# Performance work log

Measured on AMD Instinct MI355X. Metric: run time of the kernel, lower is better.

## Reference

```python
import jax, jax.numpy as jnp
import numpy as np

D_MODEL = 1024; D_STATE = 64; HEADDIM = 64; EXPAND = 2
D_INNER = EXPAND * D_MODEL            # 2048
NHEADS = D_INNER // HEADDIM           # 32
NGROUPS = 1
GN = NGROUPS * D_STATE                # 64
CONV_DIM = D_INNER + 2 * (2 * GN)     # 2304
D_IN_PROJ = 2 * D_INNER + 2 * (2 * GN) + 2 * NHEADS  # 4416
K_SP = 7; K_TP = 4; CHUNK = 256
BATCH = 2; FRAMES = 8; SPATIAL = 256; SEQLEN = SPATIAL * FRAMES  # 2048


def silu(x):
    return x * jax.nn.sigmoid(x)


def flip_frames(x, f):
    # 'b (l f) d -> b l f d' flip frame axis, flatten back
    b, L, d = x.shape
    return x.reshape(b, L // f, f, d)[:, :, ::-1, :].reshape(b, L, d)


def depthwise_conv1d(x, w, b, pad):
    # x: (N, L, C), w: (C, K) depthwise, pad=(lo,hi) -> (N, L_out, C)
    y = jax.lax.conv_general_dilated(
        jnp.transpose(x, (0, 2, 1)), w[:, None, :], (1,), [pad],
        feature_group_count=w.shape[0])
    return jnp.transpose(y + b[None, :, None], (0, 2, 1))


def setup_inputs():
    rng = np.random.default_rng(0)
    f32 = lambda *s: jnp.asarray(rng.standard_normal(s), jnp.float32)
    # dt_bias init exactly as in the torch module
    dt = np.exp(rng.random(NHEADS) * (np.log(0.1) - np.log(0.001)) + np.log(0.001))
    dt = np.clip(dt, 1e-4, None)
    inv_dt = dt + np.log(-np.expm1(-dt))
    return {
        "u": f32(BATCH, SEQLEN, D_MODEL),
        "in_proj_w": f32(D_IN_PROJ, D_MODEL) * 0.02,
        "conv_sp_w": f32(CONV_DIM, K_SP) * 0.2,
        "conv_sp_b": f32(CONV_DIM) * 0.02,
        "conv_tp_w": f32(CONV_DIM, K_TP) * 0.2,
        "conv_tp_b": f32(CONV_DIM) * 0.02,
        "dt_bias": jnp.asarray(inv_dt, jnp.float32),
        "A_log": jnp.zeros((NHEADS,), jnp.float32),
        "D": jnp.ones((NHEADS,), jnp.float32),
        "fc_D_w": f32(NHEADS, D_INNER) * 0.02,
        "norm_w": jnp.ones((D_INNER,), jnp.float32),
        "out_proj_w": f32(D_MODEL, D_INNER) * 0.02,
        "num_frames": FRAMES,
    }


def chunked_scan(xh, dt, A, Bm, Cm, sp, cs):
    # xh:(R,L,h,p) dt:(R,L,h) Bm,Cm:(R,L,n). ngroups=1.
    # seq_idx semantics: rows [0:b) one segment; rows [b:2b) reset every sp tokens.
    R, L, H, P = xh.shape
    nch = L // cs
    b = R // 2
    xch = xh.reshape(R, nch, cs, H, P)
    dtc = jnp.transpose(dt.reshape(R, nch, cs, H), (0, 1, 3, 2))   # (R,nch,h,cs)
    Bch = Bm.reshape(R, nch, cs, D_STATE)
    Cch = Cm.reshape(R, nch, cs, D_STATE)
    a = dtc * A[None, None, :, None]                               # negative logs
    cum = jnp.cumsum(a, axis=-1)                                   # inclusive
    mask = jnp.tril(jnp.ones((cs, cs), bool))
    seg = cum[..., :, None] - cum[..., None, :]                    # (R,nch,h,t,s)
    Lmat = jnp.where(mask, jnp.exp(jnp.where(mask, seg, 0.0)), 0.0)
    CB = jnp.einsum('rctn,rcsn->rcts', Cch, Bch)
    M = CB[:, :, None] * Lmat * dtc[:, :, :, None, :]
    Y_intra = jnp.einsum('rchts,rcshp->rcthp', M, xch)
    # chunk-final states and cross-chunk recurrence
    G = jnp.exp(cum[..., -1:] - cum) * dtc                         # (R,nch,h,cs)
    S_chunk = jnp.einsum('rchs,rcshp,rcsn->rchpn', G, xch, Bch)
    chunk_decay = jnp.exp(cum[..., -1])                            # (R,nch,h)
    cidx = jnp.arange(nch)
    rb = (cidx > 0) & ((cidx * cs) % sp == 0)
    resetc = jnp.concatenate([jnp.zeros((b, nch), bool),
                              jnp.broadcast_to(rb, (b, nch))], axis=0)

    def cstep(S, inp):
        dec, Sc, r = inp
        S = jnp.where(r[:, None, None, None], 0.0, S)
        prev = S
        S = dec[:, :, None, None] * S + Sc
        return S, prev

    S0 = jnp.zeros((R, H, P, D_STATE), xh.dtype)
    _, prevs = jax.lax.scan(
        cstep, S0,
        (jnp.transpose(chunk_decay, (1, 0, 2)),
         jnp.transpose(S_chunk, (1, 0, 2, 3, 4)),
         resetc.T))
    prev_states = jnp.transpose(prevs, (1, 0, 2, 3, 4))            # (R,nch,h,p,n)
    Y_inter = jnp.einsum('rcht,rctn,rchpn->rcthp', jnp.exp(cum), Cch, prev_states)
    return (Y_intra + Y_inter).reshape(R, L, H, P)


def reference(u, in_proj_w, conv_sp_w, conv_sp_b, conv_tp_w, conv_tp_b,
              dt_bias, A_log, D, fc_D_w, norm_w, out_proj_w, num_frames):
    batch, seqlen, _ = u.shape
    f = num_frames
    sp = seqlen // f
    zxbcdt = u @ in_proj_w.T
    z = zxbcdt[..., :D_INNER]
    xBC = zxbcdt[..., D_INNER:D_INNER + CONV_DIM]
    dt_raw = zxbcdt[..., D_INNER + CONV_DIM:]
    dt = jnp.concatenate([dt_raw[..., :NHEADS],
                          flip_frames(dt_raw[..., NHEADS:], f)], axis=0)
    dt = jax.nn.softplus(dt + dt_bias)                             # (2b,L,h)
    A = -jnp.exp(A_log)
    # spatial depthwise conv over spatial dim per frame ('same' pad) + SiLU
    xBC = xBC.reshape(batch, sp, f, CONV_DIM).transpose(0, 2, 1, 3).reshape(batch * f, sp, CONV_DIM)
    xBC = silu(depthwise_conv1d(xBC, conv_sp_w, conv_sp_b, (K_SP // 2, K_SP // 2)))
    # causal temporal depthwise conv over frame dim per spatial location + SiLU
    xBC = xBC.reshape(batch, f, sp, CONV_DIM).transpose(0, 2, 1, 3).reshape(batch * sp, f, CONV_DIM)
    xBC = silu(depthwise_conv1d(xBC, conv_tp_w, conv_tp_b, (K_TP - 1, 0)))
    xBC = xBC.reshape(batch, seqlen, CONV_DIM)
    x = xBC[..., :D_INNER]
    BC = xBC[..., D_INNER:]
    x_orig = x
    x2 = jnp.concatenate([x, flip_frames(x, f)], axis=0)
    BC2 = jnp.concatenate([BC[..., :2 * GN], flip_frames(BC[..., 2 * GN:], f)], axis=0)
    Bm, Cm = BC2[..., :GN], BC2[..., GN:]
    xh = x2.reshape(2 * batch, seqlen, NHEADS, HEADDIM)
    y = chunked_scan(xh, dt, A, Bm, Cm, sp, CHUNK)                 # (2b,L,h,p)
    y_fwd = y[:batch].reshape(batch, seqlen, D_INNER)
    y_rev = y[batch:].reshape(batch, sp, f, D_INNER)
    # roll-by-one with zeroed first position (fwd: token axis, rev: spatial axis)
    y_fwd = jnp.concatenate([jnp.zeros_like(y_fwd[:, :1]), y_fwd[:, :-1]], axis=1)
    y_rev = jnp.concatenate([jnp.zeros_like(y_rev[:, :1]), y_rev[:, :-1]], axis=1)
    y_rev = y_rev[:, :, ::-1, :].reshape(batch, seqlen, D_INNER)
    x_res = x_orig * jnp.repeat(x_orig @ fc_D_w.T + D, HEADDIM, axis=-1)
    y = y_fwd + y_rev + x_res
    # gated RMSNorm (norm_before_gate=True): rmsnorm(y)*w*silu(z)
    y = y * jax.lax.rsqrt(jnp.mean(jnp.square(y), axis=-1, keepdims=True) + 1e-5)
    y = y * norm_w * silu(z)
    return y @ out_proj_w.T
```

## Files before the change

kernel.cpp:

```cpp
#include <hip/hip_runtime.h>
#include <hip/hip_bf16.h>
#include <math.h>

#define D_STATE   64
#define HEADDIM   64
#define D_INNER   2048
#define NHEADS    32
#define GN        64
#define CONV_DIM  2304
#define D_IN_PROJ 4416
#define ZLD       4352
#define K_SP      7
#define K_TP      4
#define CHUNK     256
#define BATCHN    2
#define FRAMES    8
#define SPATIAL   256
#define SEQLEN    2048
#define NCH       8
#define MTOT      4096

typedef __attribute__((ext_vector_type(8))) short short8;
typedef __attribute__((ext_vector_type(8))) unsigned short ushort8v;
typedef __attribute__((ext_vector_type(4))) float floatx4;

__device__ __forceinline__ float silu_f(float x) { return x / (1.f + __expf(-x)); }
__device__ __forceinline__ int flip_l(int l) { return (l & ~7) | (7 - (l & 7)); }
__device__ __forceinline__ unsigned short f2bf(float f) {
  unsigned int u = __float_as_uint(f);
  unsigned int r = (u + 0x7fffu + ((u >> 16) & 1u)) >> 16;
  return (unsigned short)r;
}
__device__ __forceinline__ float bf2f(unsigned short s) {
  return __uint_as_float(((unsigned int)s) << 16);
}
__device__ __forceinline__ unsigned int cvtpk_bf16(float lo, float hi) {
  unsigned int r;
  asm("v_cvt_pk_bf16_f32 %0, %1, %2" : "=v"(r) : "v"(lo), "v"(hi));
  return r;
}
typedef union { short8 v; unsigned int u[4]; } s8u;
__device__ __forceinline__ void gload_lds16(const unsigned short* g, unsigned short* l) {
  __builtin_amdgcn_global_load_lds((const __attribute__((address_space(1))) void*)g,
                                   (__attribute__((address_space(3))) void*)l, 16, 0, 0);
}

__global__ __launch_bounds__(256) void cast4_bf16_kernel(const float* __restrict__ a,
                                                         unsigned short* __restrict__ oa,
                                                         int na,
                                                         const float* __restrict__ b,
                                                         unsigned short* __restrict__ ob,
                                                         int nb,
                                                         const float* __restrict__ c,
                                                         unsigned short* __restrict__ oc,
                                                         int nc,
                                                         const float* __restrict__ d,
                                                         unsigned short* __restrict__ od) {
  int bid = blockIdx.x;
  const float* in;
  unsigned short* out;
  size_t blk;
  if (bid < na)                 { in = a; out = oa; blk = bid; }
  else if (bid < na + nb)       { in = b; out = ob; blk = bid - na; }
  else if (bid < na + nb + nc)  { in = c; out = oc; blk = bid - na - nb; }
  else                          { in = d; out = od; blk = bid - na - nb - nc; }
  size_t i = (blk * 256 + threadIdx.x) * 4;
  float4 v = *(const float4*)(in + i);
  ushort4 o;
  o.x = f2bf(v.x); o.y = f2bf(v.y); o.z = f2bf(v.z); o.w = f2bf(v.w);
  *(ushort4*)(out + i) = o;
}

__device__ __forceinline__ void ts_body_bf16(const unsigned short* __restrict__ A, int lda,
                                             const unsigned short* __restrict__ B, int ldb,
                                             float* __restrict__ C, int ldc, int N, int K,
                                             int m0, float* red) {
  const int tid = threadIdx.x;
  const int lane = tid & 63;
  const int w = tid >> 6;
  const int fr = lane & 15;
  const int kq = (lane >> 4) * 8;
  const int nt = N >> 4;
  const int kseg = K >> 2;
  const int k0 = w * kseg;
  floatx4 acc[4] = {};
  for (int k = k0; k < k0 + kseg; k += 32) {
    short8 af = *(const short8*)(A + (size_t)(m0 + fr) * lda + k + kq);
    for (int j = 0; j < nt; ++j) {
      short8 bf8 = *(const short8*)(B + (size_t)(j * 16 + fr) * ldb + k + kq);
      acc[j] = __builtin_amdgcn_mfma_f32_16x16x32_bf16(af, bf8, acc[j], 0, 0, 0);
    }
  }
  const int rg = (lane >> 4) * 4;
  for (int j = 0; j < nt; ++j)
#pragma unroll
    for (int q = 0; q < 4; ++q)
      red[w * 1024 + j * 256 + (rg + q) * 16 + fr] = acc[j][q];
  __syncthreads();
  const int entries = nt * 256;
  for (int e = tid; e < entries; e += 256) {
    float s = red[e] + red[1024 + e] + red[2048 + e] + red[3072 + e];
    int j = e >> 8, idx = e & 255, row = idx >> 4, col = idx & 15;
    C[(size_t)(m0 + row) * ldc + j * 16 + col] = s;
  }
}

__global__ __launch_bounds__(256) void gemm_main_kernel(
    const unsigned short* __restrict__ A, int lda,
    const unsigned short* __restrict__ B, int ldb,
    unsigned short* __restrict__ C, int ldc, int K,
    const unsigned short* __restrict__ Bdt, float* __restrict__ DTraw) {
  __shared__ __align__(16) char smem[32768];
  const int tid = threadIdx.x;
  const int lane = tid & 63;
  const int w = tid >> 6;
  if (blockIdx.x >= 1088) {
    ts_body_bf16(A, lda, Bdt, lda, DTraw, 64, 64, K,
                 (blockIdx.x - 1088) * 16, (float*)smem);
    return;
  }
  unsigned short* As = (unsigned short*)smem;
  unsigned short* Bs = As + 128 * 64;
  const int bid = blockIdx.x;
  const int xcd = bid & 7;
  const int rp  = bid >> 3;
  const int px  = rp % 17;
  const int py  = rp / 17;
  const int m0 = ((xcd >> 1) * 8 + py) * 128;
  const int n0 = ((xcd & 1) * 17 + px) * 128;
  const int wm = (w >> 1) * 64;
  const int wn = (w & 1) * 64;
  const int lrow = lane >> 3;
  const int lperm = lane & 7;
  floatx4 acc[4][4] = {};
  for (int k0 = 0; k0 < K; k0 += 64) {
#pragma unroll
    for (int j = 0; j < 8; ++j) {
      int g = j * 4 + w;
      if (g < 16) {
        int row = g * 8 + lrow;
        int cg = (lperm ^ (row & 7)) * 8;
        gload_lds16(A + (size_t)(m0 + row) * lda + k0 + cg, &As[g * 512]);
      } else {
        int gb = g - 16;
        int row = gb * 8 + lrow;
        int cg = (lperm ^ (row & 7)) * 8;
        gload_lds16(B + (size_t)(n0 + row) * ldb + k0 + cg, &Bs[gb * 512]);
      }
    }
    __syncthreads();
    const int fr = lane & 15;
    const int kq = (lane >> 4) * 8;
#pragma unroll
    for (int kk = 0; kk < 64; kk += 32) {
      int u = (kk + kq) >> 3;
      short8 af[4], bfr[4];
#pragma unroll
      for (int i = 0; i < 4; ++i) {
        int row = wm + i * 16 + fr;
        af[i] = *(const short8*)&As[(row * 8 + (u ^ (row & 7))) * 8];
      }
#pragma unroll
      for (int j = 0; j < 4; ++j) {
        int row = wn + j * 16 + fr;
        bfr[j] = *(const short8*)&Bs[(row * 8 + (u ^ (row & 7))) * 8];
      }
#pragma unroll
      for (int i = 0; i < 4; ++i)
#pragma unroll
        for (int j = 0; j < 4; ++j)
          acc[i][j] = __builtin_amdgcn_mfma_f32_16x16x32_bf16(af[i], bfr[j], acc[i][j], 0, 0, 0);
    }
    __syncthreads();
  }
  const int fr = lane & 15;
  const int rg = (lane >> 4) * 4;
  unsigned short* Ew = &As[w * 1024];
  const int rr = lane >> 3;
  const int c8 = (lane & 7) * 8;
#pragma unroll
  for (int i = 0; i < 4; ++i) {
#pragma unroll
    for (int q = 0; q < 4; ++q)
#pragma unroll
      for (int j = 0; j < 4; ++j)
        Ew[(rg + q) * 64 + j * 16 + fr] = f2bf(acc[i][j][q]);
    ushort8v v0 = *(const ushort8v*)&Ew[rr * 64 + c8];
    ushort8v v1 = *(const ushort8v*)&Ew[(rr + 8) * 64 + c8];
    *(ushort8v*)(C + (size_t)(m0 + wm + i * 16 + rr) * ldc + n0 + wn + c8) = v0;
    *(ushort8v*)(C + (size_t)(m0 + wm + i * 16 + rr + 8) * ldc + n0 + wn + c8) = v1;
  }
}

__global__ __launch_bounds__(256) void gemm_m64_f32(
    const unsigned short* __restrict__ A, int lda,
    const unsigned short* __restrict__ B, int ldb,
    float* __restrict__ C, int ldc, int K) {
  __shared__ unsigned short As[64 * 64];
  __shared__ unsigned short Bs[128 * 64];
  const int tid = threadIdx.x;
  const int lane = tid & 63;
  const int w = tid >> 6;
  const int bid = blockIdx.x;
  const int xcd = bid & 7;
  const int q8  = bid >> 3;
  const int rsel = q8 >> 5;
  const int rp   = q8 & 31;
  const int reg  = xcd + 8 * rsel;
  const int m0 = ((reg >> 1) * 8 + (rp >> 2)) * 64;
  const int n0 = ((reg & 1) * 4 + (rp & 3)) * 128;
  const int wm = (w >> 1) * 32;
  const int wn = (w & 1) * 64;
  const int lrow = lane >> 3;
  const int lperm = lane & 7;
  floatx4 acc[2][4] = {};
  for (int k0 = 0; k0 < K; k0 += 64) {
#pragma unroll
    for (int j = 0; j < 6; ++j) {
      int g = j * 4 + w;
      if (g < 8) {
        int row = g * 8 + lrow;
        int cg = (lperm ^ (row & 7)) * 8;
        gload_lds16(A + (size_t)(m0 + row) * lda + k0 + cg, &As[g * 512]);
      } else {
        int gb = g - 8;
        int row = gb * 8 + lrow;
        int cg = (lperm ^ (row & 7)) * 8;
        gload_lds16(B + (size_t)(n0 + row) * ldb + k0 + cg, &Bs[gb * 512]);
      }
    }
    __syncthreads();
    const int fr = lane & 15;
    const int kq = (lane >> 4) * 8;
#pragma unroll
    for (int kk = 0; kk < 64; kk += 32) {
      int u = (kk + kq) >> 3;
      short8 af[2], bfr[4];
#pragma unroll
      for (int i = 0; i < 2; ++i) {
        int row = wm + i * 16 + fr;
        af[i] = *(const short8*)&As[(row * 8 + (u ^ (row & 7))) * 8];
      }
#pragma unroll
      for (int j = 0; j < 4; ++j) {
        int row = wn + j * 16 + fr;
        bfr[j] = *(const short8*)&Bs[(row * 8 + (u ^ (row & 7))) * 8];
      }
#pragma unroll
      for (int i = 0; i < 2; ++i)
#pragma unroll
        for (int j = 0; j < 4; ++j)
          acc[i][j] = __builtin_amdgcn_mfma_f32_16x16x32_bf16(af[i], bfr[j], acc[i][j], 0, 0, 0);
    }
    __syncthreads();
  }
  const int col = lane & 15;
  const int rg = (lane >> 4) * 4;
#pragma unroll
  for (int i = 0; i < 2; ++i)
#pragma unroll
    for (int j = 0; j < 4; ++j)
#pragma unroll
      for (int r = 0; r < 4; ++r)
        C[(size_t)(m0 + wm + i * 16 + rg + r) * ldc + (n0 + wn + j * 16 + col)] = acc[i][j][r];
}

__global__ __launch_bounds__(256) void fused_dtconv_kernel(
    const float* __restrict__ DTraw, const float* __restrict__ dt_bias,
    const float* __restrict__ A_log, float* __restrict__ DTt, float* __restrict__ CUMS,
    const unsigned short* __restrict__ Zb, const float* __restrict__ wsp,
    const float* __restrict__ bsp, const float* __restrict__ wtp,
    const float* __restrict__ btp, unsigned short* __restrict__ XTb) {
  __shared__ __align__(16) char smem[32768];
  const int tid = threadIdx.x;
  if (blockIdx.x < 1024) {
    float* sc = (float*)smem;
    int idx = blockIdx.x * 256 + tid;
    int l  = idx & 2047;
    int rh = idx >> 11;
    int h  = rh & 31;
    int r  = rh >> 5;
    int bi = r & 1;
    int ls = (r < 2) ? l : flip_l(l);
    int ch = (r < 2) ? h : NHEADS + h;
    float raw = DTraw[((size_t)bi * SEQLEN + ls) * 64 + ch] + dt_bias[h];
    float dtv = (raw > 20.f) ? raw : log1pf(__expf(raw));
    DTt[idx] = dtv;
    float A = -__expf(A_log[h]);
    float run = dtv * A;
    sc[tid] = run;
    __syncthreads();
#pragma unroll
    for (int ofs = 1; ofs < 256; ofs <<= 1) {
      float add = (tid >= ofs) ? sc[tid - ofs] : 0.f;
      __syncthreads();
      run += add;
      sc[tid] = run;
      __syncthreads();
    }
    CUMS[idx] = run;
  } else {
    typedef float4 xsl_t[8][32];
    xsl_t* xsl = (xsl_t*)smem;
    int bid = blockIdx.x - 1024;
    const int bx = bid % 18;
    const int by = (bid / 18) & 31;
    const int bz = bid / 576;
    const int g  = tid & 31;
    const int fr = tid >> 5;
    const int c  = bx * 128 + g * 4;
    const int s0 = by * 8;
    const int bi = bz;
    float wsp_r[4][K_SP];
#pragma unroll
    for (int ch = 0; ch < 4; ++ch)
#pragma unroll
      for (int j = 0; j < K_SP; ++j) wsp_r[ch][j] = wsp[(c + ch) * K_SP + j];
    float4 bsp4 = *(const float4*)(bsp + c);
    float4 z[14];
#pragma unroll
    for (int i = 0; i < 14; ++i) {
      int ss = s0 - 3 + i;
      if (0 <= ss && ss < SPATIAL) {
        ushort4 v = *(const ushort4*)(Zb + ((size_t)bi * SEQLEN + (ss*8 + fr)) * ZLD + D_INNER + c);
        z[i] = make_float4(bf2f(v.x), bf2f(v.y), bf2f(v.z), bf2f(v.w));
      } else {
        z[i] = make_float4(0.f, 0.f, 0.f, 0.f);
      }
    }
#pragma unroll
    for (int so = 0; so < 8; ++so) {
      float4 a = bsp4;
#pragma unroll
      for (int j = 0; j < K_SP; ++j) {
        a.x += wsp_r[0][j] * z[so + j].x;
        a.y += wsp_r[1][j] * z[so + j].y;
        a.z += wsp_r[2][j] * z[so + j].z;
        a.w += wsp_r[3][j] * z[so + j].w;
      }
      a.x = silu_f(a.x); a.y = silu_f(a.y); a.z = silu_f(a.z); a.w = silu_f(a.w);
      xsl[fr][so][g] = a;
    }
    __syncthreads();
    float wtp_r[4][K_TP];
#pragma unroll
    for (int ch = 0; ch < 4; ++ch)
#pragma unroll
      for (int j = 0; j < K_TP; ++j) wtp_r[ch][j] = wtp[(c + ch) * K_TP + j];
    float4 btp4 = *(const float4*)(btp + c);
#pragma unroll
    for (int so = 0; so < 8; ++so) {
      float4 t = btp4;
#pragma unroll
      for (int j = 0; j < K_TP; ++j) {
        int ff = fr + j - (K_TP - 1);
        if (ff >= 0) {
          float4 xv = xsl[ff][so][g];
          t.x += wtp_r[0][j] * xv.x;
          t.y += wtp_r[1][j] * xv.y;
          t.z += wtp_r[2][j] * xv.z;
          t.w += wtp_r[3][j] * xv.w;
        }
      }
      ushort4 o;
      o.x = f2bf(silu_f(t.x)); o.y = f2bf(silu_f(t.y));
      o.z = f2bf(silu_f(t.z)); o.w = f2bf(silu_f(t.w));
      *(ushort4*)(XTb + ((size_t)bi * SEQLEN + ((s0 + so)*8 + fr)) * CONV_DIM + c) = o;
    }
  }
}

__global__ __launch_bounds__(256) void fused_post_kernel(
    const unsigned short* __restrict__ XTb, const float* __restrict__ DTt,
    const float* __restrict__ CUMS, float* __restrict__ CBs,
    float* __restrict__ SCH, const unsigned short* __restrict__ FCDWb,
    float* __restrict__ FCD) {
  __shared__ __align__(16) char smem[35840];
  const int tid = threadIdx.x;
  const int bidx = blockIdx.x;
  const int lane = tid & 63;
  const int w = tid >> 6;
  if (bidx < 512) {
    unsigned short* Xs = (unsigned short*)smem;
    unsigned short* Bsm = Xs + 64 * 136;
    float* gs = (float*)(Bsm + 64 * 136);
    int c = bidx & 7;
    int h = (bidx >> 3) & 31;
    int r = bidx >> 8;
    int bi = r;
    int rh = r * NHEADS + h;
    float cl = CUMS[(size_t)rh*SEQLEN + c*CHUNK + 255];
    gs[tid] = __expf(cl - CUMS[(size_t)rh*SEQLEN + c*CHUNK + tid]) * DTt[(size_t)rh*SEQLEN + c*CHUNK + tid];
    const int fr = lane & 15;
    const int kq = (lane >> 4) * 8;
    const int sr = tid >> 3;
    const int p0 = (tid & 7) * 8;
    const int swz = (tid & 7) << 3;
    floatx4 acc[4] = {};
    for (int half = 0; half < 2; ++half) {
      __syncthreads();
#pragma unroll
      for (int P = 0; P < 4; ++P) {
        int s = P * 32 + sr;
        int l = c*CHUNK + half*128 + s;
        const unsigned short* row = XTb + ((size_t)bi*SEQLEN + l)*CONV_DIM;
        ushort8v xv = *(const ushort8v*)(row + h*HEADDIM + p0);
        ushort8v bv = *(const ushort8v*)(row + D_INNER + p0);
        float g = gs[half*128 + s];
        int cswz = s ^ swz;
#pragma unroll
        for (int q = 0; q < 8; ++q) {
          Xs[(p0 + q) * 136 + cswz] = f2bf(g * bf2f(xv[q]));
          Bsm[(p0 + q) * 136 + cswz] = bv[q];
        }
      }
      __syncthreads();
#pragma unroll
      for (int sl = 0; sl < 4; ++sl) {
        int s0 = sl * 32;
        int Ra = w*16 + fr;
        short8 af = *(const short8*)&Xs[Ra * 136 + ((s0 + kq) ^ (((Ra >> 3) & 7) << 3))];
#pragma unroll
        for (int j = 0; j < 4; ++j) {
          int Rb = j*16 + fr;
          short8 bf8 = *(const short8*)&Bsm[Rb * 136 + ((s0 + kq) ^ (((Rb >> 3) & 7) << 3))];
          acc[j] = __builtin_amdgcn_mfma_f32_16x16x32_bf16(af, bf8, acc[j], 0, 0, 0);
        }
      }
    }
    const int col = lane & 15;
    const int rg = (lane >> 4) * 4;
    size_t base = (((size_t)r*NCH + c)*NHEADS + h) * (size_t)(HEADDIM*D_STATE);
#pragma unroll
    for (int j = 0; j < 4; ++j)
#pragma unroll
      for (int q = 0; q < 4; ++q)
        SCH[base + (size_t)(w*16 + rg + q)*D_STATE + j*16 + col] = acc[j][q];
  } else if (bidx < 832) {
    const int TT0[10] = {0,1,1,2,2,2,3,3,3,3};
    const int SS0[10] = {0,0,1,0,1,2,0,1,2,3};
    int idx = bidx - 512;
    int c = idx & 7;
    int k = idx >> 3;
    int tt = k % 10;
    int r = k / 10;
    int t0 = TT0[tt] * 64;
    int s0 = SS0[tt] * 64;
    int bi = r & 1;
    int bOff = D_INNER + ((r < 2) ? 0 : 2*GN);
    int cOff = bOff + GN;
    const int fr = lane & 15;
    const int kq = (lane >> 4) * 8;
    int Lc = c * CHUNK + t0 + w * 16 + fr;
    if (r >= 2) Lc = flip_l(Lc);
    const unsigned short* crow = XTb + ((size_t)bi*SEQLEN + Lc)*CONV_DIM + cOff;
    short8 af0 = *(const short8*)(crow + kq);
    short8 af1 = *(const short8*)(crow + 32 + kq);
    floatx4 acc[4] = {};
#pragma unroll
    for (int j = 0; j < 4; ++j) {
      int Ls = c * CHUNK + s0 + j * 16 + fr;
      if (r >= 2) Ls = flip_l(Ls);
      const unsigned short* brow = XTb + ((size_t)bi*SEQLEN + Ls)*CONV_DIM + bOff;
      short8 bf0 = *(const short8*)(brow + kq);
      short8 bf1 = *(const short8*)(brow + 32 + kq);
      acc[j] = __builtin_amdgcn_mfma_f32_16x16x32_bf16(af0, bf0, acc[j], 0, 0, 0);
      acc[j] = __builtin_amdgcn_mfma_f32_16x16x32_bf16(af1, bf1, acc[j], 0, 0, 0);
    }
    const int col = lane & 15;
    const int rg = (lane >> 4) * 4;
    size_t base = (((size_t)r*NCH + c) * CHUNK) * CHUNK;
#pragma unroll
    for (int j = 0; j < 4; ++j)
#pragma unroll
      for (int q = 0; q < 4; ++q)
        CBs[base + (size_t)(t0 + w*16 + rg + q)*CHUNK + (s0 + j*16 + col)] = acc[j][q];
  } else {
    ts_body_bf16(XTb, CONV_DIM, FCDWb, 2048, FCD, 32, 32, 2048,
                 (bidx - 832) * 16, (float*)smem);
  }
}

__global__ __launch_bounds__(256) void state_combine_kernel(const float* __restrict__ SCH,
                                                            const float* __restrict__ CUMS,
                                                            float* __restrict__ SPREV) {
  int bid = blockIdx.x;
  int pq = bid & 3;
  int h = (bid >> 2) & 31;
  int r = bid >> 7;
  int tid = threadIdx.x;
  int p = pq*16 + (tid >> 4);
  int n = (tid & 15) * 4;
  float4 S = make_float4(0.f, 0.f, 0.f, 0.f);
  for (int c = 0; c < NCH; ++c) {
    size_t off = ((((size_t)r*NCH + c)*NHEADS + h)*HEADDIM + p)*D_STATE + n;
    *(float4*)(SPREV + off) = S;
    float dec = __expf(CUMS[((size_t)r*NHEADS + h)*SEQLEN + c*CHUNK + 255]);
    float4 v = *(const float4*)(SCH + off);
    S.x = dec*S.x + v.x; S.y = dec*S.y + v.y;
    S.z = dec*S.z + v.z; S.w = dec*S.w + v.w;
  }
}

#define YS_ED(S0)                                                              \
  float edv[8];                                                                \
  { float4 e0_ = *(const float4*)&ecd[(S0) + kq];                              \
    float4 e1_ = *(const float4*)&ecd[(S0) + kq + 4];                          \
    edv[0]=e0_.x; edv[1]=e0_.y; edv[2]=e0_.z; edv[3]=e0_.w;                    \
    edv[4]=e1_.x; edv[5]=e1_.y; edv[6]=e1_.z; edv[7]=e1_.w; }

#define YS_BFR(S0)                                                             \
  short8 bfr[4];                                                               \
  _Pragma("unroll")                                                            \
  for (int j = 0; j < 4; ++j) {                                                \
    int R = j * 16 + fr;                                                       \
    bfr[j] = *(const short8*)&Xt[R * 264 + (((S0) + kq) ^ (((R >> 3) & 7) << 3))]; \
  }

#define YS_MFMA4(AF, ACCROW)                                                   \
  _Pragma("unroll")                                                            \
  for (int j = 0; j < 4; ++j)                                                  \
    ACCROW[j] = __builtin_amdgcn_mfma_f32_16x16x32_bf16(AF, bfr[j], ACCROW[j], 0, 0, 0);

#define YS_AF_NOMASK(C0, C1, E)                                                \
  { af_.u[0] = cvtpk_bf16(C0.x*(E)*edv[0], C0.y*(E)*edv[1]);                   \
    af_.u[1] = cvtpk_bf16(C0.z*(E)*edv[2], C0.w*(E)*edv[3]);                   \
    af_.u[2] = cvtpk_bf16(C1.x*(E)*edv[4], C1.y*(E)*edv[5]);                   \
    af_.u[3] = cvtpk_bf16(C1.z*(E)*edv[6], C1.w*(E)*edv[7]); }

#define YS_AF_MASK(C0, C1, E, TROW)                                            \
  { float wz[8] = {C0.x,C0.y,C0.z,C0.w,C1.x,C1.y,C1.z,C1.w};                   \
    _Pragma("unroll")                                                          \
    for (int jj = 0; jj < 8; ++jj) {                                           \
      float t_ = wz[jj]*(E)*edv[jj];                                           \
      wz[jj] = (kq + jj <= (TROW)) ? t_ : 0.f; }                               \
    af_.u[0]=cvtpk_bf16(wz[0],wz[1]); af_.u[1]=cvtpk_bf16(wz[2],wz[3]);        \
    af_.u[2]=cvtpk_bf16(wz[4],wz[5]); af_.u[3]=cvtpk_bf16(wz[6],wz[7]); }

#define YS_STRIP(KS, E2, ACC)                                                  \
  {                                                                            \
    const int t0s_ = (KS) * 32;                                                \
    const float* cbr0 = CBs + cbbase + (size_t)(t0s_ + fr) * CHUNK + kq;       \
    const float* cbr1 = cbr0 + (size_t)16 * CHUNK;                             \
    float4 a0 = *(const float4*)cbr0;                                          \
    float4 a1 = *(const float4*)(cbr0 + 4);                                    \
    float4 b0 = *(const float4*)cbr1;                                          \
    float4 b1 = *(const float4*)(cbr1 + 4);                                    \
    for (int sl = 0; sl < (KS); ++sl) {                                        \
      int s0 = sl * 32;                                                        \
      float4 na0 = *(const float4*)(cbr0 + s0 + 32);                           \
      float4 na1 = *(const float4*)(cbr0 + s0 + 36);                           \
      float4 nb0 = *(const float4*)(cbr1 + s0 + 32);                           \
      float4 nb1 = *(const float4*)(cbr1 + s0 + 36);                           \
      YS_ED(s0); YS_BFR(s0);                                                   \
      s8u af_;                                                                 \
      YS_AF_NOMASK(a0, a1, (E2)[0]);                                           \
      YS_MFMA4(af_.v, ACC[0]);                                                 \
      YS_AF_NOMASK(b0, b1, (E2)[1]);                                           \
      YS_MFMA4(af_.v, ACC[1]);                                                 \
      a0 = na0; a1 = na1; b0 = nb0; b1 = nb1;                                  \
    }                                                                          \
    {                                                                          \
      int s0 = (KS) * 32;                                                      \
      YS_ED(s0); YS_BFR(s0);                                                   \
      s8u af_;                                                                 \
      YS_AF_MASK(a0, a1, (E2)[0], fr);                                         \
      YS_MFMA4(af_.v, ACC[0]);                                                 \
      YS_AF_MASK(b0, b1, (E2)[1], 16 + fr);                                    \
      YS_MFMA4(af_.v, ACC[1]);                                                 \
    }                                                                          \
  }

#define YS_INTER(T0S, E2, ACC)                                                 \
  _Pragma("unroll")                                                            \
  for (int i = 0; i < 2; ++i) {                                                \
    int t = (T0S) + i * 16 + fr;                                               \
    const unsigned short* crow = XTb + ((size_t)bi*SEQLEN + c*CHUNK + t)*CONV_DIM + D_INNER + GN + n0 + kq; \
    ushort4 c0 = *(const ushort4*)crow;                                        \
    ushort4 c1 = *(const ushort4*)(crow + 4);                                  \
    float eI = (E2)[i];                                                        \
    s8u af_;                                                                   \
    af_.u[0] = cvtpk_bf16(bf2f(c0.x)*eI, bf2f(c0.y)*eI);                       \
    af_.u[1] = cvtpk_bf16(bf2f(c0.z)*eI, bf2f(c0.w)*eI);                       \
    af_.u[2] = cvtpk_bf16(bf2f(c1.x)*eI, bf2f(c1.y)*eI);                       \
    af_.u[3] = cvtpk_bf16(bf2f(c1.z)*eI, bf2f(c1.w)*eI);                       \
    YS_MFMA4(af_.v, ACC[i]);                                                   \
  }

#define YS_EPI(T0S, ACC)                                                       \
  _Pragma("unroll")                                                            \
  for (int i = 0; i < 2; ++i) {                                                \
    _Pragma("unroll")                                                          \
    for (int q = 0; q < 4; ++q)                                                \
      _Pragma("unroll")                                                        \
      for (int j = 0; j < 4; ++j)                                              \
        Ew[(rg + q) * 64 + j * 16 + fr] = f2bf(ACC[i][j][q]);                  \
    ushort8v v0 = *(const ushort8v*)&Ew[rr * 64 + c8];                         \
    ushort8v v1 = *(const ushort8v*)&Ew[(rr + 8) * 64 + c8];                   \
    *(ushort8v*)(Yb16 + ybase + (size_t)((T0S) + i*16 + rr) * D_INNER + c8) = v0;      \
    *(ushort8v*)(Yb16 + ybase + (size_t)((T0S) + i*16 + rr + 8) * D_INNER + c8) = v1;  \
  }

__global__ __launch_bounds__(256, 4) void yscan_kernel(const unsigned short* __restrict__ XTb,
                                                       const float* __restrict__ DTt,
                                                       const float* __restrict__ CUMS,
                                                       const float* __restrict__ CBs,
                                                       const float* __restrict__ SPREV,
                                                       unsigned short* __restrict__ Yb16) {
  __shared__ unsigned short Xt[64 * 264];
  __shared__ float cums[CHUNK];
  __shared__ float ecd[CHUNK];
  int tid = threadIdx.x;
  int lane = tid & 63;
  int w = tid >> 6;
  int id = blockIdx.x;
  int c = id & 7;
  int h = (id >> 3) & 31;
  int r = id >> 8;
  int rh = r * NHEADS + h;
  int bi = r & 1;
  {
    int sr = tid >> 3;
    int p0 = (tid & 7) * 8;
    int swz = (tid & 7) << 3;
#pragma unroll
    for (int P = 0; P < 8; ++P) {
      int s = P * 32 + sr;
      int L = c * CHUNK + s;
      if (r >= 2) L = flip_l(L);
      ushort8v v = *(const ushort8v*)(XTb + ((size_t)bi * SEQLEN + L) * CONV_DIM + h * HEADDIM + p0);
      int cswz = s ^ swz;
#pragma unroll
      for (int q = 0; q < 8; ++q)
        Xt[(p0 + q) * 264 + cswz] = v[q];
    }
    float cv = CUMS[(size_t)rh * SEQLEN + c * CHUNK + tid];
    cums[tid] = cv;
    ecd[tid] = __expf(-cv) * DTt[(size_t)rh * SEQLEN + c * CHUNK + tid];
  }
  __syncthreads();
  const int fr = lane & 15;
  const int kq = (lane >> 4) * 8;
  const int kA = w, kB = 7 - w;
  const int tA = kA * 32, tB = kB * 32;
  float eAr[2], eBr[2];
#pragma unroll
  for (int i = 0; i < 2; ++i) {
    eAr[i] = __expf(cums[tA + i * 16 + fr]);
    eBr[i] = __expf(cums[tB + i * 16 + fr]);
  }
  floatx4 accA[2][4] = {};
  floatx4 accB[2][4] = {};
  size_t cbbase = (((size_t)r * NCH + c) * CHUNK) * CHUNK;
  YS_STRIP(kA, eAr, accA);
  YS_STRIP(kB, eBr, accB);
  if (r < 2) {
    const float* spbase = SPREV + (((size_t)r*NCH + c)*NHEADS + h) * (size_t)(HEADDIM*D_STATE);
#pragma unroll
    for (int ns = 0; ns < 2; ++ns) {
      int n0 = ns * 32;
      short8 bfr[4];
#pragma unroll
      for (int j = 0; j < 4; ++j) {
        const float* sp = spbase + (size_t)(j*16 + fr)*D_STATE + n0 + kq;
        float4 s0v = *(const float4*)sp;
        float4 s1v = *(const float4*)(sp + 4);
        s8u bb;
        bb.u[0] = cvtpk_bf16(s0v.x, s0v.y);
        bb.u[1] = cvtpk_bf16(s0v.z, s0v.w);
        bb.u[2] = cvtpk_bf16(s1v.x, s1v.y);
        bb.u[3] = cvtpk_bf16(s1v.z, s1v.w);
        bfr[j] = bb.v;
      }
      YS_INTER(tA, eAr, accA);
      YS_INTER(tB, eBr, accB);
    }
  }
  __syncthreads();
  unsigned short* Ew = Xt + w * 1024;
  const int rg = (lane >> 4) * 4;
  const int rr = lane >> 3;
  const int c8 = (lane & 7) * 8;
  size_t ybase = ((size_t)r*SEQLEN + c*CHUNK)*D_INNER + h*HEADDIM;
  YS_EPI(tA, accA);
  YS_EPI(tB, accB);
}

__global__ __launch_bounds__(256) void combine_kernel(const unsigned short* __restrict__ Y,
                                                      const unsigned short* __restrict__ XTb,
                                                      const float* __restrict__ FCD,
                                                      const float* __restrict__ Dp,
                                                      const unsigned short* __restrict__ Zb,
                                                      const float* __restrict__ norm_w,
                                                      unsigned short* __restrict__ YPb) {
  __shared__ float red4[4];
  int row = blockIdx.x;
  int bi = row >> 11;
  int l = row & 2047;
  int s = l >> 3, fr = l & 7;
  int tid = threadIdx.x;
  int d0 = tid * 8;
  const unsigned short* yf = (l >= 1) ? Y + ((size_t)bi*SEQLEN + (l-1))*D_INNER + d0 : nullptr;
  const unsigned short* yr = (s >= 1) ? Y + ((size_t)(2+bi)*SEQLEN + ((s-1)*8 + (7-fr)))*D_INNER + d0 : nullptr;
  const unsigned short* xr = XTb + ((size_t)row)*CONV_DIM + d0;
  float fcv = FCD[(size_t)row*NHEADS + (d0 >> 6)] + Dp[d0 >> 6];
  ushort8v xv8 = *(const ushort8v*)xr;
  float v[8];
#pragma unroll
  for (int q = 0; q < 8; ++q) v[q] = bf2f(xv8[q]) * fcv;
  if (yf) {
    ushort8v a = *(const ushort8v*)yf;
#pragma unroll
    for (int q = 0; q < 8; ++q) v[q] += bf2f(a[q]);
  }
  if (yr) {
    ushort8v a = *(const ushort8v*)yr;
#pragma unroll
    for (int q = 0; q < 8; ++q) v[q] += bf2f(a[q]);
  }
  float ss = 0.f;
#pragma unroll
  for (int q = 0; q < 8; ++q) ss += v[q] * v[q];
#pragma unroll
  for (int d = 1; d < 64; d <<= 1) ss += __shfl_xor(ss, d, 64);
  if ((tid & 63) == 0) red4[tid >> 6] = ss;
  __syncthreads();
  float tot = red4[0] + red4[1] + red4[2] + red4[3];
  float rs = rsqrtf(tot / (float)D_INNER + 1e-5f);
  ushort8v zv8 = *(const ushort8v*)(Zb + ((size_t)row)*ZLD + d0);
  float4 nw0 = *(const float4*)(norm_w + d0);
  float4 nw1 = *(const float4*)(norm_w + d0 + 4);
  float nw[8] = {nw0.x,nw0.y,nw0.z,nw0.w,nw1.x,nw1.y,nw1.z,nw1.w};
  ushort8v o;
#pragma unroll
  for (int q = 0; q < 8; ++q)
    o[q] = f2bf(v[q] * rs * nw[q] * silu_f(bf2f(zv8[q])));
  *(ushort8v*)(YPb + (size_t)row*D_INNER + d0) = o;
}

extern "C" void kernel_launch(void* const* d_in, const int* in_sizes, int n_in,
                              void* d_out, int out_size, void* d_ws, size_t ws_size,
                              hipStream_t stream) {
  (void)in_sizes; (void)n_in; (void)out_size; (void)ws_size;
  const float* u          = (const float*)d_in[0];
  const float* in_proj_w  = (const float*)d_in[1];
  const float* conv_sp_w  = (const float*)d_in[2];
  const float* conv_sp_b  = (const float*)d_in[3];
  const float* conv_tp_w  = (const float*)d_in[4];
  const float* conv_tp_b  = (const float*)d_in[5];
  const float* dt_bias    = (const float*)d_in[6];
  const float* A_log      = (const float*)d_in[7];
  const float* Dp         = (const float*)d_in[8];
  const float* fc_D_w     = (const float*)d_in[9];
  const float* norm_w     = (const float*)d_in[10];
  const float* out_proj_w = (const float*)d_in[11];
  float* out = (float*)d_out;
  float* ws = (float*)d_ws;

  float* Z     = ws;
  float* SH    = Z     + 17825792ULL;
  float* XT    = SH    + 9437184ULL;
  float* DTt   = XT    + 9437184ULL;
  float* Yb    = DTt   + 262144ULL;
  float* SPREV = Yb    + 16777216ULL;
  float* FCD   = SPREV + 2097152ULL;
  float* DTraw = FCD   + 131072ULL;
  float* CUMS  = DTraw + 262144ULL;

  unsigned short* Zb   = (unsigned short*)Z;
  unsigned short* XTb  = (unsigned short*)XT;
  unsigned short* Yb16 = (unsigned short*)Yb;
  unsigned short* Ub   = (unsigned short*)Yb;
  unsigned short* Wb   = (unsigned short*)Yb + 4194304ULL;
  float* SCH = Yb + 8388608ULL;
  unsigned short* Wob = (unsigned short*)(Yb + 10485760ULL);
  unsigned short* FCDWb = (unsigned short*)(Yb + 11534336ULL);
  unsigned short* YPb = (unsigned short*)SH;

  cast4_bf16_kernel<<<10624, 256, 0, stream>>>(u, Ub, 4096, in_proj_w, Wb, 4416,
                                               out_proj_w, Wob, 2048, fc_D_w, FCDWb);
  gemm_main_kernel<<<dim3(1344), 256, 0, stream>>>(Ub, 1024, Wb, 1024, Zb, ZLD, 1024,
                                                   Wb + 4352ULL*1024, DTraw);
  fused_dtconv_kernel<<<2176, 256, 0, stream>>>(DTraw, dt_bias, A_log, DTt, CUMS,
                                                Zb, conv_sp_w, conv_sp_b,
                                                conv_tp_w, conv_tp_b, XTb);
  fused_post_kernel<<<1088, 256, 0, stream>>>(XTb, DTt, CUMS, SH, SCH, FCDWb, FCD);
  state_combine_kernel<<<256, 256, 0, stream>>>(SCH, CUMS, SPREV);
  yscan_kernel<<<dim3(1024), 256, 0, stream>>>(XTb, DTt, CUMS, SH, SPREV, Yb16);
  combine_kernel<<<4096, 256, 0, stream>>>(Yb16, XTb, FCD, Dp, Zb, norm_w, YPb);
  gemm_m64_f32<<<dim3(512), 256, 0, stream>>>(YPb, 2048, Wob, 2048, out, 1024, 2048);
}
```

Before: 275.1 us.

## Fuse chunk-state accumulation and inter-chunk combine into fused_post_kernel

The per-chunk state computation, previously spread over 512 blocks (one per row, head and chunk), now runs in 64 blocks (one per row and head). Each block loops over the 8 chunks sequentially, carries the running state in registers and writes SPREV directly, with software prefetch of the next half-chunk's loads. This removes the separate state_combine_kernel launch and the SCH round trip through global memory. In exchange the state part has much less parallelism and a serial chain over 8 chunks, which may become the critical path of this kernel.

```diff
diff --git a/kernel.cpp b/kernel.cpp
--- a/kernel.cpp
+++ b/kernel.cpp
@@ -373,73 +373,102 @@
 __global__ __launch_bounds__(256) void fused_post_kernel(
     const unsigned short* __restrict__ XTb, const float* __restrict__ DTt,
     const float* __restrict__ CUMS, float* __restrict__ CBs,
-    float* __restrict__ SCH, const unsigned short* __restrict__ FCDWb,
+    float* __restrict__ SPREV, const unsigned short* __restrict__ FCDWb,
     float* __restrict__ FCD) {
   __shared__ __align__(16) char smem[35840];
   const int tid = threadIdx.x;
   const int bidx = blockIdx.x;
   const int lane = tid & 63;
   const int w = tid >> 6;
-  if (bidx < 512) {
+  if (bidx < 64) {
     unsigned short* Xs = (unsigned short*)smem;
     unsigned short* Bsm = Xs + 64 * 136;
     float* gs = (float*)(Bsm + 64 * 136);
-    int c = bidx & 7;
-    int h = (bidx >> 3) & 31;
-    int r = bidx >> 8;
+    int h = bidx & 31;
+    int r = bidx >> 5;
     int bi = r;
     int rh = r * NHEADS + h;
-    float cl = CUMS[(size_t)rh*SEQLEN + c*CHUNK + 255];
-    gs[tid] = __expf(cl - CUMS[(size_t)rh*SEQLEN + c*CHUNK + tid]) * DTt[(size_t)rh*SEQLEN + c*CHUNK + tid];
     const int fr = lane & 15;
     const int kq = (lane >> 4) * 8;
     const int sr = tid >> 3;
     const int p0 = (tid & 7) * 8;
     const int swz = (tid & 7) << 3;
-    floatx4 acc[4] = {};
-    for (int half = 0; half < 2; ++half) {
-      __syncthreads();
-#pragma unroll
-      for (int P = 0; P < 4; ++P) {
-        int s = P * 32 + sr;
-        int l = c*CHUNK + half*128 + s;
-        const unsigned short* row = XTb + ((size_t)bi*SEQLEN + l)*CONV_DIM;
-        ushort8v xv = *(const ushort8v*)(row + h*HEADDIM + p0);
-        ushort8v bv = *(const ushort8v*)(row + D_INNER + p0);
-        float g = gs[half*128 + s];
-        int cswz = s ^ swz;
-#pragma unroll
-        for (int q = 0; q < 8; ++q) {
-          Xs[(p0 + q) * 136 + cswz] = f2bf(g * bf2f(xv[q]));
-          Bsm[(p0 + q) * 136 + cswz] = bv[q];
-        }
-      }
-      __syncthreads();
-#pragma unroll
-      for (int sl = 0; sl < 4; ++sl) {
-        int s0 = sl * 32;
-        int Ra = w*16 + fr;
-        short8 af = *(const short8*)&Xs[Ra * 136 + ((s0 + kq) ^ (((Ra >> 3) & 7) << 3))];
-#pragma unroll
-        for (int j = 0; j < 4; ++j) {
-          int Rb = j*16 + fr;
-          short8 bf8 = *(const short8*)&Bsm[Rb * 136 + ((s0 + kq) ^ (((Rb >> 3) & 7) << 3))];
-          acc[j] = __builtin_amdgcn_mfma_f32_16x16x32_bf16(af, bf8, acc[j], 0, 0, 0);
-        }
-      }
-    }
     const int col = lane & 15;
     const int rg = (lane >> 4) * 4;
-    size_t base = (((size_t)r*NCH + c)*NHEADS + h) * (size_t)(HEADDIM*D_STATE);
-#pragma unroll
-    for (int j = 0; j < 4; ++j)
-#pragma unroll
-      for (int q = 0; q < 4; ++q)
-        SCH[base + (size_t)(w*16 + rg + q)*D_STATE + j*16 + col] = acc[j][q];
-  } else if (bidx < 832) {
+    floatx4 S[4] = {};
+    floatx4 acc[4] = {};
+    ushort8v xcur[4], bcur[4], xnxt[4], bnxt[4];
+#pragma unroll
+    for (int P = 0; P < 4; ++P) {
+      int l = P * 32 + sr;
+      const unsigned short* row = XTb + ((size_t)bi*SEQLEN + l)*CONV_DIM;
+      xcur[P] = *(const ushort8v*)(row + h*HEADDIM + p0);
+      bcur[P] = *(const ushort8v*)(row + D_INNER + p0);
+    }
+    for (int c = 0; c < NCH; ++c) {
+      float cl = CUMS[(size_t)rh*SEQLEN + c*CHUNK + 255];
+      gs[tid] = __expf(cl - CUMS[(size_t)rh*SEQLEN + c*CHUNK + tid]) * DTt[(size_t)rh*SEQLEN + c*CHUNK + tid];
+      {
+        size_t base = (((size_t)r*NCH + c)*NHEADS + h) * (size_t)(HEADDIM*D_STATE);
+#pragma unroll
+        for (int j = 0; j < 4; ++j)
+#pragma unroll
+          for (int q = 0; q < 4; ++q)
+            SPREV[base + (size_t)(w*16 + rg + q)*D_STATE + j*16 + col] = S[j][q];
+      }
+      for (int hf = 0; hf < 2; ++hf) {
+        __syncthreads();
+#pragma unroll
+        for (int P = 0; P < 4; ++P) {
+          int s = P * 32 + sr;
+          float g = gs[hf*128 + s];
+          int cswz = s ^ swz;
+#pragma unroll
+          for (int q = 0; q < 8; ++q) {
+            Xs[(p0 + q) * 136 + cswz] = f2bf(g * bf2f(xcur[P][q]));
+            Bsm[(p0 + q) * 136 + cswz] = bcur[P][q];
+          }
+        }
+        {
+          int tn = c*2 + hf + 1; if (tn > 15) tn = 15;
+          int cn = tn >> 1, hn = tn & 1;
+#pragma unroll
+          for (int P = 0; P < 4; ++P) {
+            int l = cn*CHUNK + hn*128 + P*32 + sr;
+            const unsigned short* row = XTb + ((size_t)bi*SEQLEN + l)*CONV_DIM;
+            xnxt[P] = *(const ushort8v*)(row + h*HEADDIM + p0);
+            bnxt[P] = *(const ushort8v*)(row + D_INNER + p0);
+          }
+        }
+        __syncthreads();
+#pragma unroll
+        for (int sl = 0; sl < 4; ++sl) {
+          int s0 = sl * 32;
+          int Ra = w*16 + fr;
+          short8 af = *(const short8*)&Xs[Ra * 136 + ((s0 + kq) ^ (((Ra >> 3) & 7) << 3))];
+#pragma unroll
+          for (int j = 0; j < 4; ++j) {
+            int Rb = j*16 + fr;
+            short8 bf8 = *(const short8*)&Bsm[Rb * 136 + ((s0 + kq) ^ (((Rb >> 3) & 7) << 3))];
+            acc[j] = __builtin_amdgcn_mfma_f32_16x16x32_bf16(af, bf8, acc[j], 0, 0, 0);
+          }
+        }
+#pragma unroll
+        for (int P = 0; P < 4; ++P) { xcur[P] = xnxt[P]; bcur[P] = bnxt[P]; }
+      }
+      float dec = __expf(cl);
+#pragma unroll
+      for (int j = 0; j < 4; ++j)
+#pragma unroll
+        for (int q = 0; q < 4; ++q) {
+          S[j][q] = dec * S[j][q] + acc[j][q];
+          acc[j][q] = 0.f;
+        }
+    }
+  } else if (bidx < 384) {
     const int TT0[10] = {0,1,1,2,2,2,3,3,3,3};
     const int SS0[10] = {0,0,1,0,1,2,0,1,2,3};
-    int idx = bidx - 512;
+    int idx = bidx - 64;
     int c = idx & 7;
     int k = idx >> 3;
     int tt = k % 10;
@@ -477,28 +506,7 @@
         CBs[base + (size_t)(t0 + w*16 + rg + q)*CHUNK + (s0 + j*16 + col)] = acc[j][q];
   } else {
     ts_body_bf16(XTb, CONV_DIM, FCDWb, 2048, FCD, 32, 32, 2048,
-                 (bidx - 832) * 16, (float*)smem);
-  }
-}
-
-__global__ __launch_bounds__(256) void state_combine_kernel(const float* __restrict__ SCH,
-                                                            const float* __restrict__ CUMS,
-                                                            float* __restrict__ SPREV) {
-  int bid = blockIdx.x;
-  int pq = bid & 3;
-  int h = (bid >> 2) & 31;
-  int r = bid >> 7;
-  int tid = threadIdx.x;
-  int p = pq*16 + (tid >> 4);
-  int n = (tid & 15) * 4;
-  float4 S = make_float4(0.f, 0.f, 0.f, 0.f);
-  for (int c = 0; c < NCH; ++c) {
-    size_t off = ((((size_t)r*NCH + c)*NHEADS + h)*HEADDIM + p)*D_STATE + n;
-    *(float4*)(SPREV + off) = S;
-    float dec = __expf(CUMS[((size_t)r*NHEADS + h)*SEQLEN + c*CHUNK + 255]);
-    float4 v = *(const float4*)(SCH + off);
-    S.x = dec*S.x + v.x; S.y = dec*S.y + v.y;
-    S.z = dec*S.z + v.z; S.w = dec*S.w + v.w;
+                 (bidx - 384) * 16, (float*)smem);
   }
 }
 
@@ -772,7 +780,6 @@
   unsigned short* Yb16 = (unsigned short*)Yb;
   unsigned short* Ub   = (unsigned short*)Yb;
   unsigned short* Wb   = (unsigned short*)Yb + 4194304ULL;
-  float* SCH = Yb + 8388608ULL;
   unsigned short* Wob = (unsigned short*)(Yb + 10485760ULL);
   unsigned short* FCDWb = (unsigned short*)(Yb + 11534336ULL);
   unsigned short* YPb = (unsigned short*)SH;
@@ -784,8 +791,7 @@
   fused_dtconv_kernel<<<2176, 256, 0, stream>>>(DTraw, dt_bias, A_log, DTt, CUMS,
                                                 Zb, conv_sp_w, conv_sp_b,
                                                 conv_tp_w, conv_tp_b, XTb);
-  fused_post_kernel<<<1088, 256, 0, stream>>>(XTb, DTt, CUMS, SH, SCH, FCDWb, FCD);
-  state_combine_kernel<<<256, 256, 0, stream>>>(SCH, CUMS, SPREV);
+  fused_post_kernel<<<640, 256, 0, stream>>>(XTb, DTt, CUMS, SH, SPREV, FCDWb, FCD);
   yscan_kernel<<<dim3(1024), 256, 0, stream>>>(XTb, DTt, CUMS, SH, SPREV, Yb16);
   combine_kernel<<<4096, 256, 0, stream>>>(Yb16, XTb, FCD, Dp, Zb, norm_w, YPb);
   gemm_m64_f32<<<dim3(512), 256, 0, stream>>>(YPb, 2048, Wob, 2048, out, 1024, 2048);
```

Result: slower. 284.0 us (+3.3%).
